# Kernel optimization log

Measured on AMD Instinct MI355X. Metric: run time of the kernel, lower is better.

## Reference

```python
import jax, jax.numpy as jnp
import numpy as np

N_NODES = 100000
N_EDGES = 3200000
N_GRAPHS = 64
IN_DIM = 128
EDGE_DIM = 16
HIDDEN = 64
LATENT = 16


def setup_inputs() -> dict:
    key = jax.random.key(0)
    ks = jax.random.split(key, 12)
    x = jax.random.normal(ks[0], (N_NODES, IN_DIM), dtype=jnp.float32)
    edge_feat = jax.random.normal(ks[1], (N_EDGES, EDGE_DIM), dtype=jnp.float32)
    src = jax.random.randint(ks[2], (N_EDGES,), 0, N_NODES)
    dst = jax.random.randint(ks[3], (N_EDGES,), 0, N_NODES)
    node_graph = jnp.sort(jax.random.randint(ks[4], (N_NODES,), 0, N_GRAPHS))
    s = lambda d: 1.0 / np.sqrt(d)
    W1 = jax.random.normal(ks[5], (IN_DIM, HIDDEN), dtype=jnp.float32) * s(IN_DIM)
    b1 = jnp.zeros((HIDDEN,), jnp.float32)
    W2 = jax.random.normal(ks[6], (HIDDEN, HIDDEN), dtype=jnp.float32) * s(HIDDEN)
    b2 = jnp.zeros((HIDDEN,), jnp.float32)
    We = jax.random.normal(ks[7], (EDGE_DIM, HIDDEN), dtype=jnp.float32) * s(EDGE_DIM)
    be = jnp.zeros((HIDDEN,), jnp.float32)
    Wmu = jax.random.normal(ks[8], (HIDDEN, LATENT), dtype=jnp.float32) * s(HIDDEN)
    bmu = jnp.zeros((LATENT,), jnp.float32)
    Wlv = jax.random.normal(ks[9], (HIDDEN, LATENT), dtype=jnp.float32) * s(HIDDEN)
    blv = jnp.zeros((LATENT,), jnp.float32)
    return {"x": x, "edge_feat": edge_feat, "src": src, "dst": dst,
            "node_graph": node_graph, "W1": W1, "b1": b1, "W2": W2, "b2": b2,
            "We": We, "be": be, "Wmu": Wmu, "bmu": bmu, "Wlv": Wlv, "blv": blv}


def _graph_conv(h, src, dst, W, b):
    # DGL GraphConv with norm='both', allow_zero_in_degree=True, ReLU activation.
    ones = jnp.ones((src.shape[0],), h.dtype)
    deg_out = jnp.clip(jax.ops.segment_sum(ones, src, num_segments=N_NODES), 1.0)
    deg_in = jnp.clip(jax.ops.segment_sum(ones, dst, num_segments=N_NODES), 1.0)
    # project first (cheaper when out <= in), then symmetric-normalized SpMM
    hw = h @ W  # [N, out]
    hw = hw * (deg_out ** -0.5)[:, None]
    agg = jax.ops.segment_sum(hw[src], dst, num_segments=N_NODES)
    agg = agg * (deg_in ** -0.5)[:, None]
    return jax.nn.relu(agg + b)


def reference(x, edge_feat, src, dst, node_graph, W1, b1, W2, b2, We, be,
              Wmu, bmu, Wlv, blv):
    h = _graph_conv(x, src, dst, W1, b1)
    h = _graph_conv(h, src, dst, W2, b2)
    # edge_fc is computed and stored in edata in the original, but does not
    # affect the (mu, logvar) outputs
    edge_h = edge_feat @ We + be  # noqa: F841 (kept for fidelity)
    # dgl.mean_nodes: per-graph mean of node features
    sums = jax.ops.segment_sum(h, node_graph, num_segments=N_GRAPHS)
    counts = jnp.clip(jax.ops.segment_sum(jnp.ones((N_NODES,), h.dtype),
                                          node_graph, num_segments=N_GRAPHS), 1.0)
    h_graph = sums / counts[:, None]  # [G, HIDDEN]
    mu = h_graph @ Wmu + bmu
    logvar = h_graph @ Wlv + blv
    return (mu, logvar)
```

## Files before the change

kernel.cpp:

```cpp
#include <hip/hip_runtime.h>
#include <hip/hip_fp16.h>

#define N_NODES 100000
#define N_EDGES 3200000
#define N_GRAPHS 64
#define IN_DIM 128
#define HIDDEN 64
#define LATENT 16

#define NB 1024
#define BSH 7
#define NB_USED 782
#define SC_BLOCKS 256
#define NKEYS 1024
#define NBLK_AGG 1563
#define SEG_INTS (1565 * 64)

__global__ __launch_bounds__(256) void zero_k(int4* __restrict__ p, int n4) {
  int i = blockIdx.x * 256 + threadIdx.x;
  if (i < n4) p[i] = make_int4(0, 0, 0, 0);
}

__global__ __launch_bounds__(256) void hist_c_k(const int4* __restrict__ src4,
                                                const int4* __restrict__ dst4,
                                                int* __restrict__ bc_src,
                                                int* __restrict__ bc_dst,
                                                int* __restrict__ tbl_src,
                                                int* __restrict__ tbl_dst) {
  __shared__ int hs[NB], hd[NB];
  int t = threadIdx.x;
  for (int i = t; i < NB; i += 256) { hs[i] = 0; hd[i] = 0; }
  __syncthreads();
  const int Q = N_EDGES / 4;
  const int QPB = Q / SC_BLOCKS;
  int q0 = blockIdx.x * QPB, q1 = q0 + QPB;
  for (int i = q0 + t; i < q1; i += 256) {
    int4 s = src4[i], d = dst4[i];
    atomicAdd(&hs[s.x >> BSH], 1); atomicAdd(&hs[s.y >> BSH], 1);
    atomicAdd(&hs[s.z >> BSH], 1); atomicAdd(&hs[s.w >> BSH], 1);
    atomicAdd(&hd[d.x >> BSH], 1); atomicAdd(&hd[d.y >> BSH], 1);
    atomicAdd(&hd[d.z >> BSH], 1); atomicAdd(&hd[d.w >> BSH], 1);
  }
  __syncthreads();
  for (int i = t; i < NB; i += 256) {
    int a = hs[i], b = hd[i];
    tbl_src[blockIdx.x * NB + i] = a;
    tbl_dst[blockIdx.x * NB + i] = b;
    if (a) atomicAdd(&bc_src[i], a);
    if (b) atomicAdd(&bc_dst[i], b);
  }
}

__global__ __launch_bounds__(256) void scan_c_k(const int* __restrict__ bc_src,
                                                const int* __restrict__ bc_dst,
                                                int* __restrict__ bbase_src,
                                                int* __restrict__ bbase_dst) {
  __shared__ int ts[256];
  int t = threadIdx.x;
  int b4 = 4 * t;
  {
    int a0 = bc_src[b4], a1 = bc_src[b4 + 1], a2 = bc_src[b4 + 2], a3 = bc_src[b4 + 3];
    int s = a0 + a1 + a2 + a3;
    ts[t] = s;
    __syncthreads();
    for (int off = 1; off < 256; off <<= 1) {
      int x = 0;
      if (t >= off) x = ts[t - off];
      __syncthreads();
      if (t >= off) ts[t] += x;
      __syncthreads();
    }
    int run = ts[t] - s;
    bbase_src[b4] = run;
    bbase_src[b4 + 1] = run + a0;
    bbase_src[b4 + 2] = run + a0 + a1;
    bbase_src[b4 + 3] = run + a0 + a1 + a2;
    if (t == 255) bbase_src[NB] = ts[255];
    __syncthreads();
  }
  {
    int a0 = bc_dst[b4], a1 = bc_dst[b4 + 1], a2 = bc_dst[b4 + 2], a3 = bc_dst[b4 + 3];
    int s = a0 + a1 + a2 + a3;
    ts[t] = s;
    __syncthreads();
    for (int off = 1; off < 256; off <<= 1) {
      int x = 0;
      if (t >= off) x = ts[t - off];
      __syncthreads();
      if (t >= off) ts[t] += x;
      __syncthreads();
    }
    int run = ts[t] - s;
    bbase_dst[b4] = run;
    bbase_dst[b4 + 1] = run + a0;
    bbase_dst[b4 + 2] = run + a0 + a1;
    bbase_dst[b4 + 3] = run + a0 + a1 + a2;
    if (t == 255) bbase_dst[NB] = ts[255];
  }
}

__global__ __launch_bounds__(256) void scatter_c_k(const int4* __restrict__ src4,
                                                   const int4* __restrict__ dst4,
                                                   const int* __restrict__ bbase_src,
                                                   const int* __restrict__ bbase_dst,
                                                   const int* __restrict__ tbl_src,
                                                   const int* __restrict__ tbl_dst,
                                                   int* __restrict__ cur_src,
                                                   int* __restrict__ cur_dst,
                                                   int* __restrict__ sortedS,
                                                   int* __restrict__ sortedE) {
  __shared__ int rs[NB], rd[NB];
  int t = threadIdx.x;
  for (int i = t; i < NB; i += 256) {
    int a = tbl_src[blockIdx.x * NB + i];
    int b = tbl_dst[blockIdx.x * NB + i];
    rs[i] = a ? (atomicAdd(&cur_src[i], a) + bbase_src[i]) : 0;
    rd[i] = b ? (atomicAdd(&cur_dst[i], b) + bbase_dst[i]) : 0;
  }
  __syncthreads();
  const int Q = N_EDGES / 4;
  const int QPB = Q / SC_BLOCKS;
  int q0 = blockIdx.x * QPB, q1 = q0 + QPB;
  for (int i = q0 + t; i < q1; i += 256) {
    int4 s = src4[i], d = dst4[i];
    int sv[4] = {s.x, s.y, s.z, s.w};
    int dv[4] = {d.x, d.y, d.z, d.w};
#pragma unroll
    for (int k = 0; k < 4; k++) {
      int ps = atomicAdd(&rs[sv[k] >> BSH], 1);
      sortedS[ps] = sv[k];
      int pd = atomicAdd(&rd[dv[k] >> BSH], 1);
      sortedE[pd] = ((dv[k] & 127) << 17) | sv[k];
    }
  }
}

__global__ __launch_bounds__(256) void fine_sort_k(const int* __restrict__ sortedE,
                                                   const int* __restrict__ bbase_dst,
                                                   int* __restrict__ deg_in,
                                                   int* __restrict__ seg,
                                                   int* __restrict__ eblk) {
  __shared__ int hist[NKEYS];
  __shared__ int cur[NKEYS];
  __shared__ int ts[256];
  int bk = blockIdx.x, t = threadIdx.x;
  int node0 = bk << BSH;
  int e0 = bbase_dst[bk], e1 = bbase_dst[bk + 1];
  for (int i = t; i < NKEYS; i += 256) hist[i] = 0;
  __syncthreads();
  for (int j = e0 + t; j < e1; j += 256) {
    int v = sortedE[j];
    int d7 = v >> 17, sr = v & 0x1FFFF;
    int key = ((d7 >> 6) << 9) | ((sr >> 14) << 6) | ((d7 & 7) << 3) | ((d7 >> 3) & 7);
    atomicAdd(&hist[key], 1);
  }
  __syncthreads();
  int b4 = 4 * t;
  int a0 = hist[b4], a1 = hist[b4 + 1], a2 = hist[b4 + 2], a3 = hist[b4 + 3];
  int s = a0 + a1 + a2 + a3;
  ts[t] = s;
  __syncthreads();
  for (int off = 1; off < 256; off <<= 1) {
    int x = 0;
    if (t >= off) x = ts[t - off];
    __syncthreads();
    if (t >= off) ts[t] += x;
    __syncthreads();
  }
  int run = ts[t] - s;
  cur[b4] = run;
  cur[b4 + 1] = run + a0;
  cur[b4 + 2] = run + a0 + a1;
  cur[b4 + 3] = run + a0 + a1 + a2;
  __syncthreads();
  if (t < 128) {
    int n = node0 + t;
    if (n < N_NODES) {
      int sub = t >> 6, o = t & 7, row = (t >> 3) & 7;
      int base = (sub << 9) | (o << 3) | row;
      int dg = 0;
#pragma unroll
      for (int c = 0; c < 8; c++) dg += hist[base + (c << 6)];
      deg_in[n] = dg;
    }
  }
  if (t < 128) {
    int sub = t >> 6, c = (t >> 3) & 7, o = t & 7;
    seg[(bk * 2 + sub) * 64 + c * 8 + o] = e0 + cur[(sub << 9) | (c << 6) | (o << 3)];
  }
  __syncthreads();
  for (int j = e0 + t; j < e1; j += 256) {
    int v = sortedE[j];
    int d7 = v >> 17, sr = v & 0x1FFFF;
    int key = ((d7 >> 6) << 9) | ((sr >> 14) << 6) | ((d7 & 7) << 3) | ((d7 >> 3) & 7);
    int pos = e0 + atomicAdd(&cur[key], 1);
    eblk[pos] = ((d7 & 63) << 17) | sr;
  }
}

__global__ __launch_bounds__(256) void degout_c_k(const int* __restrict__ sortedS,
                                                  const int* __restrict__ bbase_src,
                                                  const int* __restrict__ node_graph,
                                                  int* __restrict__ deg_out,
                                                  float* __restrict__ counts) {
  __shared__ int h[128];
  __shared__ int hg[N_GRAPHS];
  int bk = blockIdx.x, t = threadIdx.x;
  if (t < 128) h[t] = 0;
  if (t < N_GRAPHS) hg[t] = 0;
  __syncthreads();
  int s0 = bbase_src[bk], s1 = bbase_src[bk + 1];
  for (int j = s0 + t; j < s1; j += 256) atomicAdd(&h[sortedS[j] & 127], 1);
  if (t < 128) {
    int n = (bk << BSH) | t;
    if (n < N_NODES) atomicAdd(&hg[node_graph[n]], 1);
  }
  __syncthreads();
  if (t < 128) {
    int n = (bk << BSH) | t;
    if (n < N_NODES) deg_out[n] = h[t];
  }
  if (t < N_GRAPHS && hg[t]) atomicAdd(&counts[t], (float)hg[t]);
}

__global__ __launch_bounds__(256) void gemm1_k(const float* __restrict__ X,
                                               const float* __restrict__ W,
                                               const int* __restrict__ deg,
                                               __half* __restrict__ out) {
  __shared__ float ws[IN_DIM][HIDDEN];
  int t = threadIdx.x;
  int row0_blk = blockIdx.x * 64;

  for (int i = t; i < IN_DIM * HIDDEN / 4; i += 256)
    ((float4*)ws)[i] = ((const float4*)W)[i];
  __syncthreads();

  int w = t >> 6, lane = t & 63;
  int rg = lane >> 4, cg = lane & 15;
  int r0 = w * 16 + rg * 4;
  int c0 = cg * 4;
  int row_base = row0_blk + r0;
  bool full = (row_base + 3 < N_NODES);

  float acc[4][4];
#pragma unroll
  for (int i = 0; i < 4; i++)
#pragma unroll
    for (int j = 0; j < 4; j++) acc[i][j] = 0.f;

  const float zero4[4] = {0.f, 0.f, 0.f, 0.f};
#pragma unroll 4
  for (int d4 = 0; d4 < IN_DIM / 4; d4++) {
    float4 a0, a1, a2, a3;
    if (full) {
      a0 = *(const float4*)&X[(size_t)(row_base + 0) * IN_DIM + d4 * 4];
      a1 = *(const float4*)&X[(size_t)(row_base + 1) * IN_DIM + d4 * 4];
      a2 = *(const float4*)&X[(size_t)(row_base + 2) * IN_DIM + d4 * 4];
      a3 = *(const float4*)&X[(size_t)(row_base + 3) * IN_DIM + d4 * 4];
    } else {
      a0 = (row_base + 0 < N_NODES) ? *(const float4*)&X[(size_t)(row_base + 0) * IN_DIM + d4 * 4] : *(const float4*)zero4;
      a1 = (row_base + 1 < N_NODES) ? *(const float4*)&X[(size_t)(row_base + 1) * IN_DIM + d4 * 4] : *(const float4*)zero4;
      a2 = (row_base + 2 < N_NODES) ? *(const float4*)&X[(size_t)(row_base + 2) * IN_DIM + d4 * 4] : *(const float4*)zero4;
      a3 = (row_base + 3 < N_NODES) ? *(const float4*)&X[(size_t)(row_base + 3) * IN_DIM + d4 * 4] : *(const float4*)zero4;
    }
#pragma unroll
    for (int dd = 0; dd < 4; dd++) {
      float4 b = *(const float4*)&ws[d4 * 4 + dd][c0];
      float av0 = (&a0.x)[dd], av1 = (&a1.x)[dd], av2 = (&a2.x)[dd], av3 = (&a3.x)[dd];
      acc[0][0] += av0 * b.x; acc[0][1] += av0 * b.y; acc[0][2] += av0 * b.z; acc[0][3] += av0 * b.w;
      acc[1][0] += av1 * b.x; acc[1][1] += av1 * b.y; acc[1][2] += av1 * b.z; acc[1][3] += av1 * b.w;
      acc[2][0] += av2 * b.x; acc[2][1] += av2 * b.y; acc[2][2] += av2 * b.z; acc[2][3] += av2 * b.w;
      acc[3][0] += av3 * b.x; acc[3][1] += av3 * b.y; acc[3][2] += av3 * b.z; acc[3][3] += av3 * b.w;
    }
  }

#pragma unroll
  for (int i = 0; i < 4; i++) {
    int row = row_base + i;
    if (row >= N_NODES) continue;
    float dg = (float)deg[row];
    if (dg < 1.f) dg = 1.f;
    float sc = rsqrtf(dg);
    __half2 p0 = __floats2half2_rn(acc[i][0] * sc, acc[i][1] * sc);
    __half2 p1 = __floats2half2_rn(acc[i][2] * sc, acc[i][3] * sc);
    union { __half2 h2[2]; float2 f2; } u;
    u.h2[0] = p0; u.h2[1] = p1;
    *(float2*)&out[(size_t)row * HIDDEN + c0] = u.f2;
  }
}

template <int MODE>
__global__ __launch_bounds__(256) void agg_seg_k(const __half* __restrict__ A,
                                                 const int* __restrict__ eblk,
                                                 const int* __restrict__ seg,
                                                 const int* __restrict__ deg_in,
                                                 const float* __restrict__ bias,
                                                 const float* __restrict__ W2,
                                                 const int* __restrict__ deg_out,
                                                 const int* __restrict__ node_graph,
                                                 float* __restrict__ sums,
                                                 __half* __restrict__ out) {
  __shared__ float acc[64][68];
  __shared__ int ngs[64];
  __shared__ float psum[4][64];
  int bk = blockIdx.x, t = threadIdx.x;
  int o = t >> 5, l = t & 31;
  for (int i = t; i < 64 * 68; i += 256) ((float*)acc)[i] = 0.f;
  __syncthreads();
  int segbase = bk * 64;
  float rx = 0.f, ry = 0.f;
  int cur_d = -1;
#pragma unroll
  for (int c = 0; c < 8; c++) {
    int j0 = seg[segbase + c * 8 + o];
    int j1 = seg[segbase + c * 8 + o + 1];
    int j = j0;
    int ev = (j + 16 <= j1) ? eblk[j + (l & 15)] : 0;
    for (; j + 16 <= j1; ) {
      int ev_cur = ev;
      int jn = j + 16;
      if (jn + 16 <= j1) ev = eblk[jn + (l & 15)];
      int vv[16];
#pragma unroll
      for (int k = 0; k < 16; k++) vv[k] = __shfl(ev_cur, k, 32);
      float2 ff[16];
#pragma unroll
      for (int k = 0; k < 16; k++)
        ff[k] = __half22float2(*(const __half2*)&A[(size_t)(vv[k] & 0x1FFFF) * HIDDEN + 2 * l]);
#pragma unroll
      for (int k = 0; k < 16; k++) {
        int d = vv[k] >> 17;
        if (d != cur_d) {
          if (cur_d >= 0) {
            float2* ap = (float2*)&acc[cur_d][2 * l];
            float2 a0 = *ap; a0.x += rx; a0.y += ry; *ap = a0;
          }
          cur_d = d; rx = 0.f; ry = 0.f;
        }
        rx += ff[k].x; ry += ff[k].y;
      }
      j = jn;
    }
    for (; j + 4 <= j1; j += 4) {
      int vv[4];
#pragma unroll
      for (int k = 0; k < 4; k++) vv[k] = eblk[j + k];
      float2 ff[4];
#pragma unroll
      for (int k = 0; k < 4; k++)
        ff[k] = __half22float2(*(const __half2*)&A[(size_t)(vv[k] & 0x1FFFF) * HIDDEN + 2 * l]);
#pragma unroll
      for (int k = 0; k < 4; k++) {
        int d = vv[k] >> 17;
        if (d != cur_d) {
          if (cur_d >= 0) {
            float2* ap = (float2*)&acc[cur_d][2 * l];
            float2 a0 = *ap; a0.x += rx; a0.y += ry; *ap = a0;
          }
          cur_d = d; rx = 0.f; ry = 0.f;
        }
        rx += ff[k].x; ry += ff[k].y;
      }
    }
    for (; j < j1; j++) {
      int v = eblk[j];
      int d = v >> 17;
      if (d != cur_d) {
        if (cur_d >= 0) {
          float2* ap = (float2*)&acc[cur_d][2 * l];
          float2 a0 = *ap; a0.x += rx; a0.y += ry; *ap = a0;
        }
        cur_d = d; rx = 0.f; ry = 0.f;
      }
      float2 f = __half22float2(*(const __half2*)&A[(size_t)(v & 0x1FFFF) * HIDDEN + 2 * l]);
      rx += f.x; ry += f.y;
    }
  }
  if (cur_d >= 0) {
    float2* ap = (float2*)&acc[cur_d][2 * l];
    float2 a0 = *ap; a0.x += rx; a0.y += ry; *ap = a0;
  }
  __syncthreads();

  int node0 = bk << 6;
  if constexpr (MODE == 1) {
    for (int i = t; i < 64 * 64; i += 256) {
      int r = i >> 6, ch = i & 63;
      float dg = (float)deg_in[node0 + r];
      if (dg < 1.f) dg = 1.f;
      float v = acc[r][ch] * rsqrtf(dg) + bias[ch];
      acc[r][ch] = v > 0.f ? v : 0.f;
    }
    __syncthreads();
    int w = t >> 6, lane = t & 63;
    int rg = lane >> 4, cg = lane & 15;
    int r0 = w * 16 + rg * 4;
    int c0 = cg * 4;
    float oacc[4][4];
#pragma unroll
    for (int i = 0; i < 4; i++)
#pragma unroll
      for (int j = 0; j < 4; j++) oacc[i][j] = 0.f;
#pragma unroll 4
    for (int d = 0; d < 64; d++) {
      float4 b = *(const float4*)&W2[d * HIDDEN + c0];
      float a0 = acc[r0 + 0][d], a1 = acc[r0 + 1][d];
      float a2 = acc[r0 + 2][d], a3 = acc[r0 + 3][d];
      oacc[0][0] += a0 * b.x; oacc[0][1] += a0 * b.y; oacc[0][2] += a0 * b.z; oacc[0][3] += a0 * b.w;
      oacc[1][0] += a1 * b.x; oacc[1][1] += a1 * b.y; oacc[1][2] += a1 * b.z; oacc[1][3] += a1 * b.w;
      oacc[2][0] += a2 * b.x; oacc[2][1] += a2 * b.y; oacc[2][2] += a2 * b.z; oacc[2][3] += a2 * b.w;
      oacc[3][0] += a3 * b.x; oacc[3][1] += a3 * b.y; oacc[3][2] += a3 * b.z; oacc[3][3] += a3 * b.w;
    }
#pragma unroll
    for (int i = 0; i < 4; i++) {
      int node = node0 + r0 + i;
      if (node >= N_NODES) continue;
      float dg = (float)deg_out[node];
      if (dg < 1.f) dg = 1.f;
      float sc = rsqrtf(dg);
      __half2 p0 = __floats2half2_rn(oacc[i][0] * sc, oacc[i][1] * sc);
      __half2 p1 = __floats2half2_rn(oacc[i][2] * sc, oacc[i][3] * sc);
      union { __half2 h2[2]; float2 f2; } u;
      u.h2[0] = p0; u.h2[1] = p1;
      *(float2*)&out[(size_t)node * HIDDEN + c0] = u.f2;
    }
  } else {
    if (t < 64) {
      int node = node0 + t;
      ngs[t] = (node < N_NODES) ? node_graph[node] : -1;
    }
    __syncthreads();
    int ch = t & 63, q = t >> 6;
    bool uniform = (ngs[0] >= 0) && (ngs[0] == ngs[63]);
    if (uniform) {
      float a = 0.f;
      for (int r = q * 16; r < q * 16 + 16; r++) {
        float dg = (float)deg_in[node0 + r];
        if (dg < 1.f) dg = 1.f;
        float v = acc[r][ch] * rsqrtf(dg) + bias[ch];
        a += (v > 0.f ? v : 0.f);
      }
      psum[q][ch] = a;
      __syncthreads();
      if (t < 64) {
        float s4 = psum[0][t] + psum[1][t] + psum[2][t] + psum[3][t];
        atomicAdd(&sums[ngs[0] * HIDDEN + t], s4);
      }
    } else {
      int curg = -1; float a = 0.f;
      for (int r = q * 16; r < q * 16 + 16; r++) {
        int g = ngs[r];
        if (g != curg) {
          if (curg >= 0) atomicAdd(&sums[curg * HIDDEN + ch], a);
          curg = g; a = 0.f;
        }
        if (g >= 0) {
          float dg = (float)deg_in[node0 + r];
          if (dg < 1.f) dg = 1.f;
          float v = acc[r][ch] * rsqrtf(dg) + bias[ch];
          a += (v > 0.f ? v : 0.f);
        }
      }
      if (curg >= 0) atomicAdd(&sums[curg * HIDDEN + ch], a);
    }
  }
}

__global__ __launch_bounds__(256) void final_k(const float* __restrict__ sums,
                                               const float* __restrict__ counts,
                                               const float* __restrict__ Wmu,
                                               const float* __restrict__ bmu,
                                               const float* __restrict__ Wlv,
                                               const float* __restrict__ blv,
                                               float* __restrict__ out) {
  __shared__ float hg[N_GRAPHS][HIDDEN];
  __shared__ float wmu[HIDDEN][LATENT];
  __shared__ float wlv[HIDDEN][LATENT];
  int t = threadIdx.x;
  for (int i = t; i < N_GRAPHS * HIDDEN; i += 256) {
    int g = i / HIDDEN;
    float c = counts[g];
    if (c < 1.f) c = 1.f;
    hg[g][i % HIDDEN] = sums[i] / c;
  }
  for (int i = t; i < HIDDEN * LATENT; i += 256) {
    wmu[i / LATENT][i % LATENT] = Wmu[i];
    wlv[i / LATENT][i % LATENT] = Wlv[i];
  }
  __syncthreads();
  for (int i = t; i < N_GRAPHS * LATENT; i += 256) {
    int g = i / LATENT, j = i % LATENT;
    float mu = bmu[j], lv = blv[j];
#pragma unroll
    for (int k = 0; k < HIDDEN; k++) {
      float v = hg[g][k];
      mu += v * wmu[k][j];
      lv += v * wlv[k][j];
    }
    out[i] = mu;
    out[N_GRAPHS * LATENT + i] = lv;
  }
}

extern "C" void kernel_launch(void* const* d_in, const int* in_sizes, int n_in,
                              void* d_out, int out_size, void* d_ws, size_t ws_size,
                              hipStream_t stream) {
  const float* x = (const float*)d_in[0];
  const int* src = (const int*)d_in[2];
  const int* dst = (const int*)d_in[3];
  const int* node_graph = (const int*)d_in[4];
  const float* W1 = (const float*)d_in[5];
  const float* b1 = (const float*)d_in[6];
  const float* W2 = (const float*)d_in[7];
  const float* b2 = (const float*)d_in[8];
  const float* Wmu = (const float*)d_in[11];
  const float* bmu = (const float*)d_in[12];
  const float* Wlv = (const float*)d_in[13];
  const float* blv = (const float*)d_in[14];
  float* out = (float*)d_out;

  char* ws = (char*)d_ws;
  int* bc_src   = (int*)(ws + 0);
  int* bc_dst   = (int*)(ws + 4096);
  int* cur_src  = (int*)(ws + 8192);
  int* cur_dst  = (int*)(ws + 12288);
  float* cnts   = (float*)(ws + 16384);
  float* sums   = (float*)(ws + 16896);
  int* bbase_src = (int*)(ws + 33280);
  int* bbase_dst = (int*)(ws + 37632);
  int* tbl_src   = (int*)(ws + 41984);
  int* tbl_dst   = (int*)(ws + 1090560);
  int* deg_out = (int*)(ws + 2139136);
  int* deg_in  = (int*)(ws + 2539264);
  int* seg     = (int*)(ws + 2939392);
  int* eblk    = (int*)(ws + 3340800);
  int* sortedS = (int*)(ws + 16140800);
  int* sortedE = (int*)(ws + 28940800);
  __half* A1   = (__half*)(ws + 16140800);
  __half* A2   = (__half*)(ws + 28940800);

  zero_k<<<(33280 / 16 + 255) / 256, 256, 0, stream>>>((int4*)ws, 33280 / 16);

  hist_c_k<<<SC_BLOCKS, 256, 0, stream>>>((const int4*)src, (const int4*)dst,
                                          bc_src, bc_dst, tbl_src, tbl_dst);
  scan_c_k<<<1, 256, 0, stream>>>(bc_src, bc_dst, bbase_src, bbase_dst);
  scatter_c_k<<<SC_BLOCKS, 256, 0, stream>>>((const int4*)src, (const int4*)dst,
                                             bbase_src, bbase_dst, tbl_src, tbl_dst,
                                             cur_src, cur_dst, sortedS, sortedE);
  fine_sort_k<<<NB_USED, 256, 0, stream>>>(sortedE, bbase_dst, deg_in, seg, eblk);
  degout_c_k<<<NB_USED, 256, 0, stream>>>(sortedS, bbase_src, node_graph, deg_out, cnts);

  const int GEMM_BLKS = (N_NODES + 63) / 64;

  gemm1_k<<<GEMM_BLKS, 256, 0, stream>>>(x, W1, deg_out, A1);
  agg_seg_k<1><<<NBLK_AGG, 256, 0, stream>>>(A1, eblk, seg, deg_in, b1, W2, deg_out,
                                             nullptr, nullptr, A2);
  agg_seg_k<2><<<NBLK_AGG, 256, 0, stream>>>(A2, eblk, seg, deg_in, b2, nullptr, nullptr,
                                             node_graph, sums, nullptr);

  final_k<<<1, 256, 0, stream>>>(sums, cnts, Wmu, bmu, Wlv, blv, out);
}
```

Measured before the change: 312.7 us.

## Pad per-row edge segments to multiples of 16 with sentinels to drop tail loops

The fine sort now pads each aggregation segment's edge list up to a multiple of 16 and fills the padding with a sentinel word pointing at a zeroed dummy node row, which moves the eblk layout and workspace offsets. The aggregation kernel then runs only the 16-wide shuffle loop, with no 4-wide or scalar tail loops, and loads the segment boundaries into LDS once per block. This removes divergent tail handling in exchange for extra gathers of the zero dummy row and slightly larger edge arrays.

```diff
diff --git a/kernel.cpp b/kernel.cpp
--- a/kernel.cpp
+++ b/kernel.cpp
@@ -14,11 +14,19 @@
 #define SC_BLOCKS 256
 #define NKEYS 1024
 #define NBLK_AGG 1563
-#define SEG_INTS (1565 * 64)
+#define SEG_STRIDE 65
+#define PAD_SLACK 1920
+#define SENT_NODE 100000
+#define SENT_WORD ((63 << 17) | SENT_NODE)
 
 __global__ __launch_bounds__(256) void zero_k(int4* __restrict__ p, int n4) {
   int i = blockIdx.x * 256 + threadIdx.x;
   if (i < n4) p[i] = make_int4(0, 0, 0, 0);
+}
+__global__ __launch_bounds__(256) void zero2_k(int4* __restrict__ a, int4* __restrict__ b) {
+  int t = threadIdx.x;
+  if (t < 128) a[t] = make_int4(0, 0, 0, 0);
+  else b[t - 128] = make_int4(0, 0, 0, 0);
 }
 
 __global__ __launch_bounds__(256) void hist_c_k(const int4* __restrict__ src4,
@@ -143,9 +151,11 @@
   __shared__ int hist[NKEYS];
   __shared__ int cur[NKEYS];
   __shared__ int ts[256];
+  __shared__ int segR[128], segP[128], segS[129];
   int bk = blockIdx.x, t = threadIdx.x;
   int node0 = bk << BSH;
   int e0 = bbase_dst[bk], e1 = bbase_dst[bk + 1];
+  int e0p = e0 + bk * PAD_SLACK;
   for (int i = t; i < NKEYS; i += 256) hist[i] = 0;
   __syncthreads();
   for (int j = e0 + t; j < e1; j += 256) {
@@ -155,24 +165,31 @@
     atomicAdd(&hist[key], 1);
   }
   __syncthreads();
-  int b4 = 4 * t;
-  int a0 = hist[b4], a1 = hist[b4 + 1], a2 = hist[b4 + 2], a3 = hist[b4 + 3];
-  int s = a0 + a1 + a2 + a3;
-  ts[t] = s;
-  __syncthreads();
-  for (int off = 1; off < 256; off <<= 1) {
+  if (t < 128) {
+    int R = 0;
+#pragma unroll
+    for (int r = 0; r < 8; r++) R += hist[8 * t + r];
+    segR[t] = R;
+    segP[t] = (R + 15) & ~15;
+  }
+  __syncthreads();
+  ts[t] = (t < 128) ? segP[t] : 0;
+  __syncthreads();
+  for (int off = 1; off < 128; off <<= 1) {
     int x = 0;
-    if (t >= off) x = ts[t - off];
-    __syncthreads();
-    if (t >= off) ts[t] += x;
-    __syncthreads();
-  }
-  int run = ts[t] - s;
-  cur[b4] = run;
-  cur[b4 + 1] = run + a0;
-  cur[b4 + 2] = run + a0 + a1;
-  cur[b4 + 3] = run + a0 + a1 + a2;
-  __syncthreads();
+    if (t >= off && t < 128) x = ts[t - off];
+    __syncthreads();
+    if (t >= off && t < 128) ts[t] += x;
+    __syncthreads();
+  }
+  if (t < 128) segS[t] = ts[t] - segP[t];
+  if (t == 127) segS[128] = ts[127];
+  __syncthreads();
+  if (t < 128) {
+    int run = segS[t];
+#pragma unroll
+    for (int r = 0; r < 8; r++) { cur[8 * t + r] = run; run += hist[8 * t + r]; }
+  }
   if (t < 128) {
     int n = node0 + t;
     if (n < N_NODES) {
@@ -185,16 +202,22 @@
     }
   }
   if (t < 128) {
-    int sub = t >> 6, c = (t >> 3) & 7, o = t & 7;
-    seg[(bk * 2 + sub) * 64 + c * 8 + o] = e0 + cur[(sub << 9) | (c << 6) | (o << 3)];
-  }
+    int sub = t >> 6;
+    seg[(bk * 2 + sub) * SEG_STRIDE + (t & 63)] = e0p + segS[t];
+  }
+  if (t == 0) seg[(bk * 2) * SEG_STRIDE + 64] = e0p + segS[64];
+  if (t == 1) seg[(bk * 2 + 1) * SEG_STRIDE + 64] = e0p + segS[128];
   __syncthreads();
   for (int j = e0 + t; j < e1; j += 256) {
     int v = sortedE[j];
     int d7 = v >> 17, sr = v & 0x1FFFF;
     int key = ((d7 >> 6) << 9) | ((sr >> 14) << 6) | ((d7 & 7) << 3) | ((d7 >> 3) & 7);
-    int pos = e0 + atomicAdd(&cur[key], 1);
+    int pos = e0p + atomicAdd(&cur[key], 1);
     eblk[pos] = ((d7 & 63) << 17) | sr;
+  }
+  if (t < 128) {
+    int s = segS[t] + segR[t], e = segS[t] + segP[t];
+    for (int i = s; i < e; i++) eblk[e0p + i] = SENT_WORD;
   }
 }
 
@@ -301,25 +324,26 @@
                                                  float* __restrict__ sums,
                                                  __half* __restrict__ out) {
   __shared__ float acc[64][68];
+  __shared__ int segLDS[SEG_STRIDE];
   __shared__ int ngs[64];
   __shared__ float psum[4][64];
   int bk = blockIdx.x, t = threadIdx.x;
   int o = t >> 5, l = t & 31;
   for (int i = t; i < 64 * 68; i += 256) ((float*)acc)[i] = 0.f;
-  __syncthreads();
-  int segbase = bk * 64;
+  if (t < SEG_STRIDE) segLDS[t] = seg[bk * SEG_STRIDE + t];
+  __syncthreads();
   float rx = 0.f, ry = 0.f;
   int cur_d = -1;
 #pragma unroll
   for (int c = 0; c < 8; c++) {
-    int j0 = seg[segbase + c * 8 + o];
-    int j1 = seg[segbase + c * 8 + o + 1];
+    int j0 = segLDS[c * 8 + o];
+    int j1 = segLDS[c * 8 + o + 1];
     int j = j0;
-    int ev = (j + 16 <= j1) ? eblk[j + (l & 15)] : 0;
-    for (; j + 16 <= j1; ) {
+    int ev = 0;
+    if (j < j1) ev = eblk[j + (l & 15)];
+    for (; j < j1; j += 16) {
       int ev_cur = ev;
-      int jn = j + 16;
-      if (jn + 16 <= j1) ev = eblk[jn + (l & 15)];
+      if (j + 16 < j1) ev = eblk[j + 16 + (l & 15)];
       int vv[16];
 #pragma unroll
       for (int k = 0; k < 16; k++) vv[k] = __shfl(ev_cur, k, 32);
@@ -339,41 +363,6 @@
         }
         rx += ff[k].x; ry += ff[k].y;
       }
-      j = jn;
-    }
-    for (; j + 4 <= j1; j += 4) {
-      int vv[4];
-#pragma unroll
-      for (int k = 0; k < 4; k++) vv[k] = eblk[j + k];
-      float2 ff[4];
-#pragma unroll
-      for (int k = 0; k < 4; k++)
-        ff[k] = __half22float2(*(const __half2*)&A[(size_t)(vv[k] & 0x1FFFF) * HIDDEN + 2 * l]);
-#pragma unroll
-      for (int k = 0; k < 4; k++) {
-        int d = vv[k] >> 17;
-        if (d != cur_d) {
-          if (cur_d >= 0) {
-            float2* ap = (float2*)&acc[cur_d][2 * l];
-            float2 a0 = *ap; a0.x += rx; a0.y += ry; *ap = a0;
-          }
-          cur_d = d; rx = 0.f; ry = 0.f;
-        }
-        rx += ff[k].x; ry += ff[k].y;
-      }
-    }
-    for (; j < j1; j++) {
-      int v = eblk[j];
-      int d = v >> 17;
-      if (d != cur_d) {
-        if (cur_d >= 0) {
-          float2* ap = (float2*)&acc[cur_d][2 * l];
-          float2 a0 = *ap; a0.x += rx; a0.y += ry; *ap = a0;
-        }
-        cur_d = d; rx = 0.f; ry = 0.f;
-      }
-      float2 f = __half22float2(*(const __half2*)&A[(size_t)(v & 0x1FFFF) * HIDDEN + 2 * l]);
-      rx += f.x; ry += f.y;
     }
   }
   if (cur_d >= 0) {
@@ -533,13 +522,16 @@
   int* deg_out = (int*)(ws + 2139136);
   int* deg_in  = (int*)(ws + 2539264);
   int* seg     = (int*)(ws + 2939392);
-  int* eblk    = (int*)(ws + 3340800);
-  int* sortedS = (int*)(ws + 16140800);
-  int* sortedE = (int*)(ws + 28940800);
-  __half* A1   = (__half*)(ws + 16140800);
-  __half* A2   = (__half*)(ws + 28940800);
+  int* eblk    = (int*)(ws + 3346176);
+  int* sortedS = (int*)(ws + 24010752);
+  int* sortedE = (int*)(ws + 36812800);
+  __half* A1   = (__half*)(ws + 24010752);
+  __half* A2   = (__half*)(ws + 36812800);
+  int4* strip1 = (int4*)(ws + 24010752 + 12800000);
+  int4* strip2 = (int4*)(ws + 36812800 + 12800000);
 
   zero_k<<<(33280 / 16 + 255) / 256, 256, 0, stream>>>((int4*)ws, 33280 / 16);
+  zero2_k<<<1, 256, 0, stream>>>(strip1, strip2);
 
   hist_c_k<<<SC_BLOCKS, 256, 0, stream>>>((const int4*)src, (const int4*)dst,
                                           bc_src, bc_dst, tbl_src, tbl_dst);
```

Result: no change. 313.5 us (+0.2%).
